# Optimization experiments

Measured on AMD Instinct MI355X. Metric: run time of the kernel, lower is better.

Reference implementation:

```python
import jax, jax.numpy as jnp
import numpy as np

N_HEADS = 8
EPS = 1e-12  # F.normalize eps


def setup_inputs() -> dict:
    key = jax.random.key(0)
    ks = jax.random.split(key, 7)
    B, M, S, D = 2, 4, 2048, 512
    scale = 1.0 / np.sqrt(D)
    return {
        "x": jax.random.normal(ks[0], (B, M, S, D), dtype=jnp.float32),
        "Wq": jax.random.normal(ks[1], (D, D), dtype=jnp.float32) * scale,
        "bq": jax.random.normal(ks[2], (D,), dtype=jnp.float32) * 0.01,
        "Wkv": jax.random.normal(ks[3], (D, D), dtype=jnp.float32) * scale,
        "bkv": jax.random.normal(ks[4], (D,), dtype=jnp.float32) * 0.01,
        "Wo": jax.random.normal(ks[5], (D, D), dtype=jnp.float32) * scale,
        "bo": jax.random.normal(ks[6], (D,), dtype=jnp.float32) * 0.01,
    }


def _heads(t, H):
    # [B,M,S,D] -> [B,M,H,S,dk]
    B, Mo, S, D = t.shape
    return t.reshape(B, Mo, S, H, D // H).swapaxes(2, 3)


def reference(x, Wq, bq, Wkv, bkv, Wo, bo):
    B, Mo, S, D = x.shape
    H = N_HEADS
    # nn.Linear: y = x @ W^T + b
    Q = x @ Wq.T + bq
    KV = x @ Wkv.T + bkv  # K and V share this projection
    Qh = _heads(Q, H)
    Kh = _heads(KV, H)
    Vh = Kh
    # L2-normalize along head dim (cosine attention)
    Qn = Qh / jnp.maximum(jnp.linalg.norm(Qh, axis=-1, keepdims=True), EPS)
    Kn = Kh / jnp.maximum(jnp.linalg.norm(Kh, axis=-1, keepdims=True), EPS)
    scores = jnp.einsum("bmhqd,bmhkd->bmhqk", Qn, Kn)
    attn = jax.nn.softmax(scores, axis=-1)  # dropout=0 (eval)
    ctx = jnp.einsum("bmhqk,bmhkd->bmhqd", attn, Vh)
    ctx = ctx.swapaxes(2, 3).reshape(B, Mo, S, D)
    return ctx @ Wo.T + bo
```

## Files before the change

### kernel.cpp

```cpp
#include <hip/hip_runtime.h>

typedef __attribute__((ext_vector_type(8))) short bf16x8;
typedef __attribute__((ext_vector_type(8))) _Float16 f16x8;
typedef __attribute__((ext_vector_type(2))) _Float16 f16x2;
typedef __attribute__((ext_vector_type(4))) float f32x4;

__device__ __forceinline__ unsigned short f2bf(float f) {
  union { float f; unsigned int i; } v;
  v.f = f;
  unsigned int r = v.i + 0x7FFFu + ((v.i >> 16) & 1u);
  return (unsigned short)(r >> 16);
}

__device__ __forceinline__ f16x2 cvt_pk(float a, float b) {
  return __builtin_bit_cast(f16x2, __builtin_amdgcn_cvt_pkrtz(a, b));
}

__device__ __forceinline__ void gl_lds16(const unsigned short* g, unsigned short* l) {
  __builtin_amdgcn_global_load_lds(
      (const __attribute__((address_space(1))) unsigned int*)g,
      (__attribute__((address_space(3))) unsigned int*)l, 16, 0, 0);
}

__device__ __forceinline__ f16x2 exp_poly(f16x2 x) {
  const f16x2 a5 = {(_Float16)0.00868682f, (_Float16)0.00868682f};
  const f16x2 a4 = {(_Float16)0.04379392f, (_Float16)0.04379392f};
  const f16x2 a3 = {(_Float16)0.16648887f, (_Float16)0.16648887f};
  const f16x2 a2 = {(_Float16)0.49919676f, (_Float16)0.49919676f};
  const f16x2 a1 = {(_Float16)1.00002229f, (_Float16)1.00002229f};
  const f16x2 a0 = {(_Float16)1.00004478f, (_Float16)1.00004478f};
#if __has_builtin(__builtin_elementwise_fma)
  f16x2 r = a5;
  r = __builtin_elementwise_fma(r, x, a4);
  r = __builtin_elementwise_fma(r, x, a3);
  r = __builtin_elementwise_fma(r, x, a2);
  r = __builtin_elementwise_fma(r, x, a1);
  r = __builtin_elementwise_fma(r, x, a0);
#else
  f16x2 r = a5;
  r = r * x + a4;
  r = r * x + a3;
  r = r * x + a2;
  r = r * x + a1;
  r = r * x + a0;
#endif
  return r;
}

__global__ __launch_bounds__(256) void cvt_all(
    const float* __restrict__ x, const float* __restrict__ wq,
    const float* __restrict__ wkv, const float* __restrict__ wo,
    unsigned short* __restrict__ xf, unsigned short* __restrict__ wqf,
    unsigned short* __restrict__ wkvf, unsigned short* __restrict__ wof) {
  int b = blockIdx.x;
  const float* in;
  unsigned short* out;
  int i;
  if (b < 8192) { in = x; out = xf; i = b * 256 + threadIdx.x; }
  else if (b < 8448) { in = wq; out = wqf; i = (b - 8192) * 256 + threadIdx.x; }
  else if (b < 8704) { in = wkv; out = wkvf; i = (b - 8448) * 256 + threadIdx.x; }
  else { in = wo; out = wof; i = (b - 8704) * 256 + threadIdx.x; }
  float4 v = ((const float4*)in)[i];
  int f = i << 2;
  int row = f >> 9, c = f & 511;
  long off = ((((long)(row >> 7) * 8 + (c >> 6)) * 16 + ((row >> 4) & 7) * 2 +
               ((c >> 5) & 1)) * 64 + ((c >> 3) & 3) * 16 + (row & 15)) * 8 + (c & 7);
  ushort4 o;
  o.x = f2bf(v.x);
  o.y = f2bf(v.y);
  o.z = f2bf(v.z);
  o.w = f2bf(v.w);
  *(ushort4*)(out + off) = o;
}

__global__ __launch_bounds__(256) void gemm_qkv(
    const unsigned short* __restrict__ xf, const unsigned short* __restrict__ Wqf,
    const unsigned short* __restrict__ Wkvf, const float* __restrict__ bq,
    const float* __restrict__ bkv, unsigned short* __restrict__ Qn,
    unsigned short* __restrict__ Kf, unsigned short* __restrict__ Vf) {
  __shared__ __attribute__((aligned(16))) unsigned short lA[16 * 512];
  __shared__ __attribute__((aligned(16))) unsigned short lB[16 * 512];
  const int isKV = (int)(blockIdx.y >> 2);
  const unsigned short* Btf = isKV ? Wkvf : Wqf;
  const float* bias = isKV ? bkv : bq;
  const int tid = threadIdx.x;
  const int lane = tid & 63;
  const int quad = lane >> 4, m16 = lane & 15;
  const int w = tid >> 6;
  const int wm = w >> 1, wn = w & 1;
  const long mb = (long)blockIdx.x * 128;
  const int nt = (int)(blockIdx.y & 3);
  const long nb = (long)nt * 128;
  f32x4 acc[4][4];
#pragma unroll
  for (int i = 0; i < 4; i++)
#pragma unroll
    for (int j = 0; j < 4; j++) acc[i][j] = (f32x4){0.f, 0.f, 0.f, 0.f};

  for (int kb = 0; kb < 8; kb++) {
    __syncthreads();
    {
      const unsigned short* gA =
          xf + (((long)blockIdx.x * 8 + kb) * 16 + 4 * w) * 512 + lane * 8;
      gl_lds16(gA, &lA[(4 * w + 0) * 512]);
      gl_lds16(gA + 512, &lA[(4 * w + 1) * 512]);
      gl_lds16(gA + 1024, &lA[(4 * w + 2) * 512]);
      gl_lds16(gA + 1536, &lA[(4 * w + 3) * 512]);
      const unsigned short* gB =
          Btf + (((long)nt * 8 + kb) * 16 + 4 * w) * 512 + lane * 8;
      gl_lds16(gB, &lB[(4 * w + 0) * 512]);
      gl_lds16(gB + 512, &lB[(4 * w + 1) * 512]);
      gl_lds16(gB + 1024, &lB[(4 * w + 2) * 512]);
      gl_lds16(gB + 1536, &lB[(4 * w + 3) * 512]);
    }
    __syncthreads();
#pragma unroll
    for (int ks = 0; ks < 2; ks++) {
      bf16x8 af[4], bfr[4];
#pragma unroll
      for (int i = 0; i < 4; i++)
        af[i] = *(const bf16x8*)&lA[(((wm * 4 + i) << 1) | ks) * 512 + lane * 8];
#pragma unroll
      for (int j = 0; j < 4; j++)
        bfr[j] = *(const bf16x8*)&lB[(((wn * 4 + j) << 1) | ks) * 512 + lane * 8];
#pragma unroll
      for (int i = 0; i < 4; i++)
#pragma unroll
        for (int j = 0; j < 4; j++)
          acc[i][j] =
              __builtin_amdgcn_mfma_f32_16x16x32_bf16(af[i], bfr[j], acc[i][j], 0, 0, 0);
    }
  }
  const int h = (int)(nb >> 6) + wn;
#pragma unroll
  for (int i = 0; i < 4; i++) {
    long row0 = mb + wm * 64 + i * 16 + quad * 4;
    float bb[4], val[4][4], inv[4];
#pragma unroll
    for (int j = 0; j < 4; j++) {
      bb[j] = bias[nb + wn * 64 + j * 16 + m16];
#pragma unroll
      for (int r = 0; r < 4; r++) val[j][r] = acc[i][j][r] + bb[j];
    }
#pragma unroll
    for (int r = 0; r < 4; r++) {
      float s = val[0][r] * val[0][r] + val[1][r] * val[1][r] +
                val[2][r] * val[2][r] + val[3][r] * val[3][r];
      s += __shfl_xor(s, 1);
      s += __shfl_xor(s, 2);
      s += __shfl_xor(s, 4);
      s += __shfl_xor(s, 8);
      inv[r] = 1.0f / fmaxf(sqrtf(s), 1e-12f);
    }
    if (!isKV) {
#pragma unroll
      for (int r = 0; r < 4; r++)
#pragma unroll
        for (int j = 0; j < 4; j++) {
          long col = nb + wn * 64 + j * 16 + m16;
          Qn[(row0 + r) * 512 + col] = f2bf(val[j][r] * inv[r]);
        }
    } else {
      const int bm = (int)(row0 >> 11);
      const int g = bm * 8 + h;
      const int kt = (int)((row0 & 2047) >> 6);
      const long tb = ((long)g * 32 + kt) * 8;
#pragma unroll
      for (int j = 0; j < 4; j++) {
        long kb0 = (tb + i * 2 + (j >> 1)) * 512 +
                   (((((j & 1) << 1) | (m16 >> 3)) * 16 + quad * 4) * 8) + (m16 & 7);
#pragma unroll
        for (int r = 0; r < 4; r++) Kf[kb0 + r * 8] = f2bf(val[j][r] * inv[r]);
      }
#pragma unroll
      for (int j = 0; j < 4; j++) {
        long vo = (tb + j * 2 + (i >> 1)) * 512 +
                  ((((((i & 1) << 1) | (quad >> 1)) * 16 + m16)) * 8) + (quad & 1) * 4;
        f16x2 lo = cvt_pk(val[j][0], val[j][1]);
        f16x2 hi = cvt_pk(val[j][2], val[j][3]);
        uint2 pk = make_uint2(__builtin_bit_cast(unsigned int, lo),
                              __builtin_bit_cast(unsigned int, hi));
        *(uint2*)(Vf + vo) = pk;
      }
    }
  }
}

__global__ __launch_bounds__(256) void gemm_o(
    const unsigned short* __restrict__ Af, const unsigned short* __restrict__ Btf,
    const float* __restrict__ bias, float* __restrict__ Cout) {
  __shared__ __attribute__((aligned(16))) unsigned short lA[16 * 512];
  __shared__ __attribute__((aligned(16))) unsigned short lB[16 * 512];
  const int tid = threadIdx.x;
  const int lane = tid & 63;
  const int quad = lane >> 4, m16 = lane & 15;
  const int w = tid >> 6;
  const int wm = w >> 1, wn = w & 1;
  const long mb = (long)blockIdx.x * 128;
  const int nt = (int)blockIdx.y;
  const long nb = (long)nt * 128;
  f32x4 acc[4][4];
#pragma unroll
  for (int i = 0; i < 4; i++)
#pragma unroll
    for (int j = 0; j < 4; j++) acc[i][j] = (f32x4){0.f, 0.f, 0.f, 0.f};

  for (int kb = 0; kb < 8; kb++) {
    __syncthreads();
    {
      const unsigned short* gA =
          Af + (((long)blockIdx.x * 8 + kb) * 16 + 4 * w) * 512 + lane * 8;
      gl_lds16(gA, &lA[(4 * w + 0) * 512]);
      gl_lds16(gA + 512, &lA[(4 * w + 1) * 512]);
      gl_lds16(gA + 1024, &lA[(4 * w + 2) * 512]);
      gl_lds16(gA + 1536, &lA[(4 * w + 3) * 512]);
      const unsigned short* gB =
          Btf + (((long)nt * 8 + kb) * 16 + 4 * w) * 512 + lane * 8;
      gl_lds16(gB, &lB[(4 * w + 0) * 512]);
      gl_lds16(gB + 512, &lB[(4 * w + 1) * 512]);
      gl_lds16(gB + 1024, &lB[(4 * w + 2) * 512]);
      gl_lds16(gB + 1536, &lB[(4 * w + 3) * 512]);
    }
    __syncthreads();
#pragma unroll
    for (int ks = 0; ks < 2; ks++) {
      bf16x8 af[4], bfr[4];
#pragma unroll
      for (int i = 0; i < 4; i++)
        af[i] = *(const bf16x8*)&lA[(((wm * 4 + i) << 1) | ks) * 512 + lane * 8];
#pragma unroll
      for (int j = 0; j < 4; j++)
        bfr[j] = *(const bf16x8*)&lB[(((wn * 4 + j) << 1) | ks) * 512 + lane * 8];
#pragma unroll
      for (int i = 0; i < 4; i++)
#pragma unroll
        for (int j = 0; j < 4; j++)
          acc[i][j] =
              __builtin_amdgcn_mfma_f32_16x16x32_bf16(af[i], bfr[j], acc[i][j], 0, 0, 0);
    }
  }
#pragma unroll
  for (int i = 0; i < 4; i++) {
    long row0 = mb + wm * 64 + i * 16 + quad * 4;
#pragma unroll
    for (int j = 0; j < 4; j++) {
      long col = nb + wn * 64 + j * 16 + m16;
      float bb = bias[col];
#pragma unroll
      for (int r = 0; r < 4; r++) Cout[(row0 + r) * 512 + col] = acc[i][j][r] + bb;
    }
  }
}

__global__ __launch_bounds__(512, 4) void attn_cos(
    const unsigned short* __restrict__ Qn, const unsigned short* __restrict__ Kf,
    const unsigned short* __restrict__ Vf, unsigned short* __restrict__ ctxf) {
  __shared__ __attribute__((aligned(16))) unsigned short lK[8 * 512];
  __shared__ __attribute__((aligned(16))) unsigned short lVt[8 * 512];
  __shared__ __attribute__((aligned(16))) unsigned short lP[256 * 64];
  const int id = (int)blockIdx.x;
  const int g = ((id >> 6) << 3) | (id & 7);
  const int qt = (id >> 3) & 7;
  const int bm = g >> 3, h = g & 7;
  const int tid = threadIdx.x;
  const int lane = tid & 63;
  const int quad = lane >> 4, m16 = lane & 15;
  const int w = tid >> 6;
  const long qrow0 = (long)bm * 2048 + qt * 256 + w * 32;
  const int colbase = h * 64;
  const int swz = (m16 & 7) << 3;
  unsigned short* myP = lP + (w * 32) * 64;

  bf16x8 qf[2][2];
#pragma unroll
  for (int i = 0; i < 2; i++)
#pragma unroll
    for (int ks = 0; ks < 2; ks++)
      qf[i][ks] = *(const bf16x8*)(Qn + (qrow0 + i * 16 + m16) * 512 + colbase +
                                   ks * 32 + quad * 8);

  f32x4 cacc[2][4];
#pragma unroll
  for (int i = 0; i < 2; i++)
#pragma unroll
    for (int j = 0; j < 4; j++) cacc[i][j] = (f32x4){0.f, 0.f, 0.f, 0.f};
  f32x4 cacc_l[2];
  cacc_l[0] = (f32x4){0.f, 0.f, 0.f, 0.f};
  cacc_l[1] = (f32x4){0.f, 0.f, 0.f, 0.f};
  const f16x8 onesv = {(_Float16)1.0f, (_Float16)1.0f, (_Float16)1.0f, (_Float16)1.0f,
                       (_Float16)1.0f, (_Float16)1.0f, (_Float16)1.0f, (_Float16)1.0f};

  for (int kt = 0; kt < 32; ++kt) {
    const long tb = ((long)g * 32 + kt) * 8;
    __syncthreads();
    gl_lds16(Kf + (tb + w) * 512 + lane * 8, &lK[w * 512]);
    gl_lds16(Vf + (tb + w) * 512 + lane * 8, &lVt[w * 512]);
    __syncthreads();

#pragma unroll
    for (int i = 0; i < 2; i++) {
      f32x4 sacc[4];
#pragma unroll
      for (int j = 0; j < 4; j++) sacc[j] = (f32x4){0.f, 0.f, 0.f, 0.f};
#pragma unroll
      for (int ks = 0; ks < 2; ++ks) {
        bf16x8 kfr[4];
#pragma unroll
        for (int j = 0; j < 4; j++)
          kfr[j] = *(const bf16x8*)&lK[((j << 1) | ks) * 512 + lane * 8];
#pragma unroll
        for (int j = 0; j < 4; j++)
          sacc[j] = __builtin_amdgcn_mfma_f32_16x16x32_bf16(kfr[j], qf[i][ks],
                                                            sacc[j], 0, 0, 0);
      }
#pragma unroll
      for (int j = 0; j < 4; j++) {
        f16x2 x01 = cvt_pk(sacc[j][0], sacc[j][1]);
        f16x2 x23 = cvt_pk(sacc[j][2], sacc[j][3]);
        f16x2 e01 = exp_poly(x01);
        f16x2 e23 = exp_poly(x23);
        uint2 pk2 = make_uint2(__builtin_bit_cast(unsigned int, e01),
                               __builtin_bit_cast(unsigned int, e23));
        *(uint2*)&myP[(i * 16 + m16) * 64 + ((j * 16 + quad * 4) ^ swz)] = pk2;
      }
#pragma unroll
      for (int ks = 0; ks < 2; ++ks) {
        f16x8 pfr = *(const f16x8*)&myP[(i * 16 + m16) * 64 +
                                        ((ks * 32 + quad * 8) ^ swz)];
        f16x8 vfr[4];
#pragma unroll
        for (int j = 0; j < 4; j++)
          vfr[j] = *(const f16x8*)&lVt[((j << 1) | ks) * 512 + lane * 8];
#pragma unroll
        for (int j = 0; j < 4; j++)
          cacc[i][j] = __builtin_amdgcn_mfma_f32_16x16x32_f16(pfr, vfr[j],
                                                              cacc[i][j], 0, 0, 0);
        cacc_l[i] =
            __builtin_amdgcn_mfma_f32_16x16x32_f16(pfr, onesv, cacc_l[i], 0, 0, 0);
      }
    }
  }

  float linv[2][4];
#pragma unroll
  for (int i = 0; i < 2; i++)
#pragma unroll
    for (int r = 0; r < 4; r++) linv[i][r] = 1.0f / cacc_l[i][r];
  const long cb0 = (((long)(bm * 16 + qt * 2 + (w >> 2)) * 8 + h) * 16);
#pragma unroll
  for (int i = 0; i < 2; i++)
#pragma unroll
    for (int j = 0; j < 4; j++) {
      long off = (cb0 + ((w & 3) * 2 + i) * 2 + (j >> 1)) * 512 +
                 (((((j & 1) << 1) | (m16 >> 3)) * 16 + quad * 4) * 8) + (m16 & 7);
#pragma unroll
      for (int r = 0; r < 4; r++)
        ctxf[off + r * 8] = f2bf(cacc[i][j][r] * linv[i][r]);
    }
}

extern "C" void kernel_launch(void* const* d_in, const int* in_sizes, int n_in,
                              void* d_out, int out_size, void* d_ws, size_t ws_size,
                              hipStream_t stream) {
  (void)in_sizes; (void)n_in; (void)out_size; (void)ws_size;
  const float* x = (const float*)d_in[0];
  const float* Wq = (const float*)d_in[1];
  const float* bq = (const float*)d_in[2];
  const float* Wkv = (const float*)d_in[3];
  const float* bkv = (const float*)d_in[4];
  const float* Wo = (const float*)d_in[5];
  const float* bo = (const float*)d_in[6];

  char* ws = (char*)d_ws;
  unsigned short* xf     = (unsigned short*)(ws);
  unsigned short* Wqf    = (unsigned short*)(ws + 16777216);
  unsigned short* Wkvf   = (unsigned short*)(ws + 17301504);
  unsigned short* Wof    = (unsigned short*)(ws + 17825792);
  unsigned short* Qn_bf  = (unsigned short*)(ws + 18350080);
  unsigned short* Kf     = (unsigned short*)(ws + 35127296);
  unsigned short* Vf     = (unsigned short*)(ws + 51904512);
  unsigned short* ctxf   = xf;

  cvt_all<<<8960, 256, 0, stream>>>(x, Wq, Wkv, Wo, xf, Wqf, Wkvf, Wof);

  gemm_qkv<<<dim3(128, 8), 256, 0, stream>>>(xf, Wqf, Wkvf, bq, bkv, Qn_bf, Kf, Vf);

  attn_cos<<<512, 512, 0, stream>>>(Qn_bf, Kf, Vf, ctxf);

  gemm_o<<<dim3(128, 4), 256, 0, stream>>>(ctxf, Wof, bo, (float*)d_out);
}
```

Measured before the change: 228.1 us.

## Double-buffer K/V tiles in LDS and batch both query subtiles per step

The attention kernel now prefetches the next K/V tile into a second LDS buffer while the current tile is computed, so only one barrier per iteration is needed instead of two. It also restructures the inner loops to process both 16-row query subtiles together, reusing each K and V fragment loaded from LDS for two MFMAs. This doubles K/V LDS usage and raises register pressure, which may hurt occupancy at the 512x4 launch bound. On the last iteration it issues a wasted wraparound prefetch.

```diff
diff --git a/kernel.cpp b/kernel.cpp
--- a/kernel.cpp
+++ b/kernel.cpp
@@ -255,8 +255,8 @@
 __global__ __launch_bounds__(512, 4) void attn_cos(
     const unsigned short* __restrict__ Qn, const unsigned short* __restrict__ Kf,
     const unsigned short* __restrict__ Vf, unsigned short* __restrict__ ctxf) {
-  __shared__ __attribute__((aligned(16))) unsigned short lK[8 * 512];
-  __shared__ __attribute__((aligned(16))) unsigned short lVt[8 * 512];
+  __shared__ __attribute__((aligned(16))) unsigned short lK[2][8 * 512];
+  __shared__ __attribute__((aligned(16))) unsigned short lVt[2][8 * 512];
   __shared__ __attribute__((aligned(16))) unsigned short lP[256 * 64];
   const int id = (int)blockIdx.x;
   const int g = ((id >> 6) << 3) | (id & 7);
@@ -290,55 +290,78 @@
   const f16x8 onesv = {(_Float16)1.0f, (_Float16)1.0f, (_Float16)1.0f, (_Float16)1.0f,
                        (_Float16)1.0f, (_Float16)1.0f, (_Float16)1.0f, (_Float16)1.0f};
 
+  {
+    const long tb0 = (long)g * 32 * 8;
+    gl_lds16(Kf + (tb0 + w) * 512 + lane * 8, &lK[0][w * 512]);
+    gl_lds16(Vf + (tb0 + w) * 512 + lane * 8, &lVt[0][w * 512]);
+  }
+  __syncthreads();
+
+  int cur = 0;
   for (int kt = 0; kt < 32; ++kt) {
-    const long tb = ((long)g * 32 + kt) * 8;
-    __syncthreads();
-    gl_lds16(Kf + (tb + w) * 512 + lane * 8, &lK[w * 512]);
-    gl_lds16(Vf + (tb + w) * 512 + lane * 8, &lVt[w * 512]);
-    __syncthreads();
-
-#pragma unroll
-    for (int i = 0; i < 2; i++) {
-      f32x4 sacc[4];
-#pragma unroll
-      for (int j = 0; j < 4; j++) sacc[j] = (f32x4){0.f, 0.f, 0.f, 0.f};
-#pragma unroll
-      for (int ks = 0; ks < 2; ++ks) {
-        bf16x8 kfr[4];
-#pragma unroll
-        for (int j = 0; j < 4; j++)
-          kfr[j] = *(const bf16x8*)&lK[((j << 1) | ks) * 512 + lane * 8];
-#pragma unroll
-        for (int j = 0; j < 4; j++)
-          sacc[j] = __builtin_amdgcn_mfma_f32_16x16x32_bf16(kfr[j], qf[i][ks],
-                                                            sacc[j], 0, 0, 0);
-      }
+    {
+      const int ktn = (kt + 1) & 31;
+      const long tbn = ((long)g * 32 + ktn) * 8;
+      gl_lds16(Kf + (tbn + w) * 512 + lane * 8, &lK[cur ^ 1][w * 512]);
+      gl_lds16(Vf + (tbn + w) * 512 + lane * 8, &lVt[cur ^ 1][w * 512]);
+    }
+
+    f32x4 sacc[2][4];
+#pragma unroll
+    for (int i = 0; i < 2; i++)
+#pragma unroll
+      for (int j = 0; j < 4; j++) sacc[i][j] = (f32x4){0.f, 0.f, 0.f, 0.f};
+#pragma unroll
+    for (int ks = 0; ks < 2; ++ks) {
+      bf16x8 kfr[4];
+#pragma unroll
+      for (int j = 0; j < 4; j++)
+        kfr[j] = *(const bf16x8*)&lK[cur][((j << 1) | ks) * 512 + lane * 8];
+#pragma unroll
+      for (int j = 0; j < 4; j++)
+#pragma unroll
+        for (int i = 0; i < 2; i++)
+          sacc[i][j] = __builtin_amdgcn_mfma_f32_16x16x32_bf16(kfr[j], qf[i][ks],
+                                                               sacc[i][j], 0, 0, 0);
+    }
+
+#pragma unroll
+    for (int i = 0; i < 2; i++)
 #pragma unroll
       for (int j = 0; j < 4; j++) {
-        f16x2 x01 = cvt_pk(sacc[j][0], sacc[j][1]);
-        f16x2 x23 = cvt_pk(sacc[j][2], sacc[j][3]);
+        f16x2 x01 = cvt_pk(sacc[i][j][0], sacc[i][j][1]);
+        f16x2 x23 = cvt_pk(sacc[i][j][2], sacc[i][j][3]);
         f16x2 e01 = exp_poly(x01);
         f16x2 e23 = exp_poly(x23);
         uint2 pk2 = make_uint2(__builtin_bit_cast(unsigned int, e01),
                                __builtin_bit_cast(unsigned int, e23));
         *(uint2*)&myP[(i * 16 + m16) * 64 + ((j * 16 + quad * 4) ^ swz)] = pk2;
       }
-#pragma unroll
-      for (int ks = 0; ks < 2; ++ks) {
-        f16x8 pfr = *(const f16x8*)&myP[(i * 16 + m16) * 64 +
-                                        ((ks * 32 + quad * 8) ^ swz)];
-        f16x8 vfr[4];
+
+#pragma unroll
+    for (int ks = 0; ks < 2; ++ks) {
+      f16x8 vfr[4];
+#pragma unroll
+      for (int j = 0; j < 4; j++)
+        vfr[j] = *(const f16x8*)&lVt[cur][((j << 1) | ks) * 512 + lane * 8];
+      f16x8 pfr[2];
+#pragma unroll
+      for (int i = 0; i < 2; i++)
+        pfr[i] = *(const f16x8*)&myP[(i * 16 + m16) * 64 +
+                                     ((ks * 32 + quad * 8) ^ swz)];
+#pragma unroll
+      for (int i = 0; i < 2; i++) {
 #pragma unroll
         for (int j = 0; j < 4; j++)
-          vfr[j] = *(const f16x8*)&lVt[((j << 1) | ks) * 512 + lane * 8];
-#pragma unroll
-        for (int j = 0; j < 4; j++)
-          cacc[i][j] = __builtin_amdgcn_mfma_f32_16x16x32_f16(pfr, vfr[j],
+          cacc[i][j] = __builtin_amdgcn_mfma_f32_16x16x32_f16(pfr[i], vfr[j],
                                                               cacc[i][j], 0, 0, 0);
         cacc_l[i] =
-            __builtin_amdgcn_mfma_f32_16x16x32_f16(pfr, onesv, cacc_l[i], 0, 0, 0);
+            __builtin_amdgcn_mfma_f32_16x16x32_f16(pfr[i], onesv, cacc_l[i], 0, 0, 0);
       }
     }
+
+    __syncthreads();
+    cur ^= 1;
   }
 
   float linv[2][4];
```

Measured after the change: 219.7 us. 3.7% less time.
